# Kernel optimization log

Measured on AMD Instinct MI355X. Metric: run time of the kernel, lower is better.

Reference implementation:

```python
import jax, jax.numpy as jnp
import numpy as np

DIM = 1024
HEADS = 16
DIM_HEAD = DIM // HEADS

def setup_inputs() -> dict:
    key = jax.random.key(0)
    k1, k2, k3 = jax.random.split(key, 3)
    x = jax.random.normal(k1, (2, 2048, DIM), dtype=jnp.float32)
    # nn.Linear(dim, 3*dim, bias=False): weight [3*dim, dim]; y = x @ W.T
    W_qkv = jax.random.normal(k2, (3 * DIM, DIM), dtype=jnp.float32) * (1.0 / np.sqrt(DIM))
    W_out = jax.random.normal(k3, (DIM, DIM), dtype=jnp.float32) * (1.0 / np.sqrt(DIM))
    return {"x": x, "W_qkv": W_qkv, "W_out": W_out}

def reference(x, W_qkv, W_out):
    b, s, _ = x.shape
    scale = DIM_HEAD ** -0.5
    qkv = x @ W_qkv.T                              # [b, s, 3*dim]
    q, k, v = jnp.split(qkv, 3, axis=-1)
    def to_heads(t):
        return t.reshape(b, s, HEADS, DIM_HEAD).transpose(0, 2, 1, 3)  # [b,h,s,d]
    q, k, v = map(to_heads, (q, k, v))
    scores = jnp.einsum('bhid,bhjd->bhij', q, k) * scale
    causal_mask = jnp.triu(jnp.ones((s, s), dtype=bool), k=1)
    scores = jnp.where(causal_mask, -jnp.inf, scores)
    attn = jax.nn.softmax(scores, axis=-1)
    out = jnp.einsum('bhij,bhjd->bhid', attn, v)
    out = out.transpose(0, 2, 1, 3).reshape(b, s, HEADS * DIM_HEAD)
    return out @ W_out.T
```

## Files before the change

### kernel.cpp

```cpp
#include <hip/hip_runtime.h>
#include <hip/hip_bf16.h>
#include <math.h>

using bf16 = __hip_bfloat16;
typedef __attribute__((ext_vector_type(8))) short bf16x8;
typedef __attribute__((ext_vector_type(4))) short bf16x4;
typedef __attribute__((ext_vector_type(4))) float f32x4;

static __device__ __forceinline__ void gl_lds16(const void* g, void* l) {
  __builtin_amdgcn_global_load_lds(
      (const __attribute__((address_space(1))) unsigned int*)g,
      (__attribute__((address_space(3))) unsigned int*)l, 16, 0, 0);
}

#define MFMA16 __builtin_amdgcn_mfma_f32_16x16x32_bf16
#define MFMA16K16 __builtin_amdgcn_mfma_f32_16x16x16bf16_1k

static __device__ __forceinline__ short f2bf(float f) {
  return (short)((__builtin_bit_cast(unsigned int, f) + 0x8000u) >> 16);
}

__global__ __launch_bounds__(256) void cvt_f32_bf16(
    const float* __restrict__ in, bf16* __restrict__ out) {
  const int i = (blockIdx.x * 256 + threadIdx.x) * 4;
  const float4 v = *(const float4*)(in + i);
  bf16x4 o;
  o.x = (short)__builtin_bit_cast(unsigned short, __float2bfloat16(v.x));
  o.y = (short)__builtin_bit_cast(unsigned short, __float2bfloat16(v.y));
  o.z = (short)__builtin_bit_cast(unsigned short, __float2bfloat16(v.z));
  o.w = (short)__builtin_bit_cast(unsigned short, __float2bfloat16(v.w));
  *(bf16x4*)(out + i) = o;
}

template <int K>
static __device__ __forceinline__ void gemm_bt_acc(
    const bf16* __restrict__ A, const bf16* __restrict__ B,
    int rowA0, int rowB0, bf16* As, bf16* Bs, f32x4 acc[4][4]) {
  const int t = threadIdx.x;
  const int w = t >> 6, l = t & 63;
  const int quad = l >> 4, l16 = l & 15;
  const int wm = (w >> 1) * 64, wn = (w & 1) * 64;
  const int c0 = t, c1 = t + 256;
  const bf16* a0 = A + (size_t)(rowA0 + (c0 >> 2)) * K + (c0 & 3) * 8;
  const bf16* a1 = A + (size_t)(rowA0 + (c1 >> 2)) * K + (c1 & 3) * 8;
  const bf16* b0 = B + (size_t)(rowB0 + (c0 >> 2)) * K + (c0 & 3) * 8;
  const bf16* b1 = B + (size_t)(rowB0 + (c1 >> 2)) * K + (c1 & 3) * 8;
  for (int k0 = 0; k0 < K; k0 += 32) {
    __syncthreads();
    gl_lds16(a0 + k0, As + c0 * 8);
    gl_lds16(a1 + k0, As + c1 * 8);
    gl_lds16(b0 + k0, Bs + c0 * 8);
    gl_lds16(b1 + k0, Bs + c1 * 8);
    __syncthreads();
    bf16x8 af[4], bg[4];
#pragma unroll
    for (int i = 0; i < 4; i++)
      af[i] = *(const bf16x8*)(As + (wm + i * 16 + l16) * 32 + quad * 8);
#pragma unroll
    for (int j = 0; j < 4; j++)
      bg[j] = *(const bf16x8*)(Bs + (wn + j * 16 + l16) * 32 + quad * 8);
#pragma unroll
    for (int i = 0; i < 4; i++)
#pragma unroll
      for (int j = 0; j < 4; j++)
        acc[i][j] = MFMA16(af[i], bg[j], acc[i][j], 0, 0, 0);
  }
}

__global__ __launch_bounds__(256) void qkv_gemm(
    const bf16* __restrict__ x, const bf16* __restrict__ Wqkv,
    bf16* __restrict__ Qb, bf16* __restrict__ Kb, bf16* __restrict__ Vt) {
  __shared__ bf16 As[128 * 32];
  __shared__ bf16 Bs[128 * 32];
  f32x4 acc[4][4];
#pragma unroll
  for (int i = 0; i < 4; i++)
#pragma unroll
    for (int j = 0; j < 4; j++) acc[i][j] = (f32x4){0.f, 0.f, 0.f, 0.f};
  const int bm = blockIdx.x, bn = blockIdx.y;
  gemm_bt_acc<1024>(x, Wqkv, bm * 128, bn * 128, As, Bs, acc);

  const int t = threadIdx.x, w = t >> 6, l = t & 63;
  const int quad = l >> 4, l16 = l & 15;
  const int wm = (w >> 1) * 64, wn = (w & 1) * 64;
#pragma unroll
  for (int i = 0; i < 4; i++) {
#pragma unroll
    for (int j = 0; j < 4; j++) {
      const int n = bn * 128 + wn + j * 16 + l16;
      const int which = n >> 10;
      const int nn = n & 1023;
      const int h = nn >> 6, d = nn & 63;
#pragma unroll
      for (int r = 0; r < 4; r++) {
        const int m = bm * 128 + wm + i * 16 + quad * 4 + r;
        const int b = m >> 11, s = m & 2047;
        const int bh = b * 16 + h;
        const bf16 v = __float2bfloat16(acc[i][j][r]);
        if (which == 0)
          Qb[((size_t)bh * 2048 + s) * 64 + d] = v;
        else if (which == 1)
          Kb[((size_t)bh * 2048 + s) * 64 + d] = v;
        else
          Vt[((size_t)bh * 64 + d) * 2048 + s] = v;
      }
    }
  }
}

__global__ __launch_bounds__(256) void attn_kernel(
    const bf16* __restrict__ Qb, const bf16* __restrict__ Kb,
    const bf16* __restrict__ Vt, bf16* __restrict__ attn) {
  __shared__ bf16 Qs[64 * 64];
  __shared__ bf16 Ks[64 * 64];
  __shared__ bf16 Vts[64 * 64];
  const int x = blockIdx.x;
  const int bh = x & 31;
  const int idx = x >> 5;
  const int qt = (idx < 16) ? idx : 47 - idx;
  const int q0 = qt * 64;
  const int t = threadIdx.x, w = t >> 6, l = t & 63;
  const int quad = l >> 4, l16 = l & 15;
  const float c_exp2 = 0.18033688011f;

  const bf16* Qg = Qb + ((size_t)bh * 2048 + q0) * 64;
#pragma unroll
  for (int c = t; c < 512; c += 256) {
    const int row = c >> 3, pos = c & 7;
    gl_lds16(Qg + (row * 8 + (pos ^ (row & 7))) * 8, Qs + c * 8);
  }

  f32x4 oacc[4];
  float lsum = 0.f;
#pragma unroll
  for (int md = 0; md < 4; md++) oacc[md] = (f32x4){0.f, 0.f, 0.f, 0.f};

  const int nj = qt + 1;
  for (int j = 0; j < nj; j++) {
    const int j0 = j * 64;
    __syncthreads();
    const bf16* Kg = Kb + ((size_t)bh * 2048 + j0) * 64;
#pragma unroll
    for (int c = t; c < 512; c += 256) {
      const int row = c >> 3, pos = c & 7;
      gl_lds16(Kg + (row * 8 + (pos ^ (row & 7))) * 8, Ks + c * 8);
    }
    const bf16* Vg = Vt + (size_t)bh * 64 * 2048 + j0;
#pragma unroll
    for (int c = t; c < 512; c += 256) {
      const int d = c >> 3, pos = c & 7;
      gl_lds16(Vg + (size_t)d * 2048 + ((pos ^ (d & 7)) * 8), Vts + c * 8);
    }
    __syncthreads();

    f32x4 sacc[4];
#pragma unroll
    for (int mt = 0; mt < 4; mt++) sacc[mt] = (f32x4){0.f, 0.f, 0.f, 0.f};
#pragma unroll
    for (int kk = 0; kk < 2; kk++) {
      const int qrow = w * 16 + l16;
      const int qpos = (kk * 4 + quad) ^ (qrow & 7);
      bf16x8 qf = *(const bf16x8*)(Qs + qrow * 64 + qpos * 8);
#pragma unroll
      for (int mt = 0; mt < 4; mt++) {
        const int row = mt * 16 + l16;
        const int pos = (kk * 4 + quad) ^ (row & 7);
        bf16x8 kf = *(const bf16x8*)(Ks + row * 64 + pos * 8);
        sacc[mt] = MFMA16(kf, qf, sacc[mt], 0, 0, 0);
      }
    }

    bf16x4 pfrag[4];
#pragma unroll
    for (int mt = 0; mt < 4; mt++) {
      bf16x4 p4;
#pragma unroll
      for (int r = 0; r < 4; r++) {
        float p = exp2f(sacc[mt][r] * c_exp2);
        if (j == qt) {
          const int sg = j0 + mt * 16 + quad * 4 + r;
          const int qi = q0 + w * 16 + l16;
          if (sg > qi) p = 0.f;
        }
        lsum += p;
        p4[r] = f2bf(p);
      }
      pfrag[mt] = p4;
    }

#pragma unroll
    for (int kt = 0; kt < 4; kt++) {
#pragma unroll
      for (int md = 0; md < 4; md++) {
        const int d = md * 16 + l16;
        const int pos = (kt * 2 + (quad >> 1)) ^ (d & 7);
        bf16x4 va = *(const bf16x4*)(Vts + d * 64 + pos * 8 + (quad & 1) * 4);
        oacc[md] = MFMA16K16(va, pfrag[kt], oacc[md], 0, 0, 0);
      }
    }
  }

  lsum += __shfl_xor(lsum, 16, 64);
  lsum += __shfl_xor(lsum, 32, 64);
  const float inv = 1.0f / lsum;
  const int b = bh >> 4, h = bh & 15;
  const int srow = q0 + w * 16 + l16;
#pragma unroll
  for (int md = 0; md < 4; md++) {
    bf16x4 o4;
#pragma unroll
    for (int r = 0; r < 4; r++)
      o4[r] = (short)__builtin_bit_cast(
          unsigned short, __float2bfloat16(oacc[md][r] * inv));
    *(bf16x4*)(attn + ((size_t)b * 2048 + srow) * 1024 + h * 64 + md * 16 +
               quad * 4) = o4;
  }
}

__global__ __launch_bounds__(256) void out_gemm(
    const bf16* __restrict__ attn, const bf16* __restrict__ Wout,
    float* __restrict__ out) {
  __shared__ bf16 As[128 * 32];
  __shared__ bf16 Bs[128 * 32];
  f32x4 acc[4][4];
#pragma unroll
  for (int i = 0; i < 4; i++)
#pragma unroll
    for (int j = 0; j < 4; j++) acc[i][j] = (f32x4){0.f, 0.f, 0.f, 0.f};
  const int bm = blockIdx.x, bn = blockIdx.y;
  gemm_bt_acc<1024>(attn, Wout, bm * 128, bn * 128, As, Bs, acc);

  const int t = threadIdx.x, w = t >> 6, l = t & 63;
  const int quad = l >> 4, l16 = l & 15;
  const int wm = (w >> 1) * 64, wn = (w & 1) * 64;
#pragma unroll
  for (int i = 0; i < 4; i++) {
#pragma unroll
    for (int j = 0; j < 4; j++) {
      const int n = bn * 128 + wn + j * 16 + l16;
#pragma unroll
      for (int r = 0; r < 4; r++) {
        const int m = bm * 128 + wm + i * 16 + quad * 4 + r;
        out[(size_t)m * 1024 + n] = acc[i][j][r];
      }
    }
  }
}

extern "C" void kernel_launch(void* const* d_in, const int* in_sizes, int n_in,
                              void* d_out, int out_size, void* d_ws, size_t ws_size,
                              hipStream_t stream) {
  const float* x = (const float*)d_in[0];
  const float* Wqkv = (const float*)d_in[1];
  const float* Wout = (const float*)d_in[2];
  float* out = (float*)d_out;

  char* ws = (char*)d_ws;
  const size_t MB = 1024 * 1024;
  bf16* xb = (bf16*)(ws + 0 * MB);
  bf16* at = (bf16*)(ws + 0 * MB);
  bf16* Wqkvb = (bf16*)(ws + 8 * MB);
  bf16* Woutb = (bf16*)(ws + 14 * MB);
  bf16* Qb = (bf16*)(ws + 16 * MB);
  bf16* Kb = (bf16*)(ws + 24 * MB);
  bf16* Vt = (bf16*)(ws + 32 * MB);

  cvt_f32_bf16<<<4096, 256, 0, stream>>>(x, xb);
  cvt_f32_bf16<<<3072, 256, 0, stream>>>(Wqkv, Wqkvb);
  cvt_f32_bf16<<<1024, 256, 0, stream>>>(Wout, Woutb);

  qkv_gemm<<<dim3(32, 24), 256, 0, stream>>>(xb, Wqkvb, Qb, Kb, Vt);
  attn_kernel<<<1024, 256, 0, stream>>>(Qb, Kb, Vt, at);
  out_gemm<<<dim3(32, 8), 256, 0, stream>>>(at, Woutb, out);
}
```

Before: 183.7 us.

## Widen attention KV tile to 128 and merge conversion kernels into one launch

```diff
diff --git a/kernel.cpp b/kernel.cpp
--- a/kernel.cpp
+++ b/kernel.cpp
@@ -20,16 +20,29 @@
   return (short)((__builtin_bit_cast(unsigned int, f) + 0x8000u) >> 16);
 }
 
-__global__ __launch_bounds__(256) void cvt_f32_bf16(
-    const float* __restrict__ in, bf16* __restrict__ out) {
-  const int i = (blockIdx.x * 256 + threadIdx.x) * 4;
-  const float4 v = *(const float4*)(in + i);
+__global__ __launch_bounds__(256) void cvt_all(
+    const float* __restrict__ x, const float* __restrict__ wqkv,
+    const float* __restrict__ wout, bf16* __restrict__ xb,
+    bf16* __restrict__ wqkvb, bf16* __restrict__ woutb) {
+  const int blk = blockIdx.x;
+  const float* src;
+  bf16* dst;
+  int base;
+  if (blk < 4096) {
+    src = x; dst = xb; base = blk;
+  } else if (blk < 7168) {
+    src = wqkv; dst = wqkvb; base = blk - 4096;
+  } else {
+    src = wout; dst = woutb; base = blk - 7168;
+  }
+  const int i = (base * 256 + threadIdx.x) * 4;
+  const float4 v = *(const float4*)(src + i);
   bf16x4 o;
-  o.x = (short)__builtin_bit_cast(unsigned short, __float2bfloat16(v.x));
-  o.y = (short)__builtin_bit_cast(unsigned short, __float2bfloat16(v.y));
-  o.z = (short)__builtin_bit_cast(unsigned short, __float2bfloat16(v.z));
-  o.w = (short)__builtin_bit_cast(unsigned short, __float2bfloat16(v.w));
-  *(bf16x4*)(out + i) = o;
+  o.x = f2bf(v.x);
+  o.y = f2bf(v.y);
+  o.z = f2bf(v.z);
+  o.w = f2bf(v.w);
+  *(bf16x4*)(dst + i) = o;
 }
 
 template <int K>
@@ -112,8 +125,8 @@
     const bf16* __restrict__ Qb, const bf16* __restrict__ Kb,
     const bf16* __restrict__ Vt, bf16* __restrict__ attn) {
   __shared__ bf16 Qs[64 * 64];
-  __shared__ bf16 Ks[64 * 64];
-  __shared__ bf16 Vts[64 * 64];
+  __shared__ bf16 Ks[128 * 64];
+  __shared__ bf16 Vts[64 * 128];
   const int x = blockIdx.x;
   const int bh = x & 31;
   const int idx = x >> 5;
@@ -135,34 +148,34 @@
 #pragma unroll
   for (int md = 0; md < 4; md++) oacc[md] = (f32x4){0.f, 0.f, 0.f, 0.f};
 
-  const int nj = qt + 1;
-  for (int j = 0; j < nj; j++) {
-    const int j0 = j * 64;
+  const int njj = (qt + 2) >> 1;
+  for (int jj = 0; jj < njj; jj++) {
+    const int j0 = jj * 128;
     __syncthreads();
     const bf16* Kg = Kb + ((size_t)bh * 2048 + j0) * 64;
 #pragma unroll
-    for (int c = t; c < 512; c += 256) {
+    for (int c = t; c < 1024; c += 256) {
       const int row = c >> 3, pos = c & 7;
       gl_lds16(Kg + (row * 8 + (pos ^ (row & 7))) * 8, Ks + c * 8);
     }
     const bf16* Vg = Vt + (size_t)bh * 64 * 2048 + j0;
 #pragma unroll
-    for (int c = t; c < 512; c += 256) {
-      const int d = c >> 3, pos = c & 7;
-      gl_lds16(Vg + (size_t)d * 2048 + ((pos ^ (d & 7)) * 8), Vts + c * 8);
-    }
-    __syncthreads();
-
-    f32x4 sacc[4];
-#pragma unroll
-    for (int mt = 0; mt < 4; mt++) sacc[mt] = (f32x4){0.f, 0.f, 0.f, 0.f};
+    for (int c = t; c < 1024; c += 256) {
+      const int d = c >> 4, pos = c & 15;
+      gl_lds16(Vg + (size_t)d * 2048 + ((pos ^ (d & 15)) * 8), Vts + c * 8);
+    }
+    __syncthreads();
+
+    f32x4 sacc[8];
+#pragma unroll
+    for (int mt = 0; mt < 8; mt++) sacc[mt] = (f32x4){0.f, 0.f, 0.f, 0.f};
 #pragma unroll
     for (int kk = 0; kk < 2; kk++) {
       const int qrow = w * 16 + l16;
       const int qpos = (kk * 4 + quad) ^ (qrow & 7);
       bf16x8 qf = *(const bf16x8*)(Qs + qrow * 64 + qpos * 8);
 #pragma unroll
-      for (int mt = 0; mt < 4; mt++) {
+      for (int mt = 0; mt < 8; mt++) {
         const int row = mt * 16 + l16;
         const int pos = (kk * 4 + quad) ^ (row & 7);
         bf16x8 kf = *(const bf16x8*)(Ks + row * 64 + pos * 8);
@@ -170,31 +183,42 @@
       }
     }
 
-    bf16x4 pfrag[4];
-#pragma unroll
-    for (int mt = 0; mt < 4; mt++) {
-      bf16x4 p4;
-#pragma unroll
-      for (int r = 0; r < 4; r++) {
-        float p = exp2f(sacc[mt][r] * c_exp2);
-        if (j == qt) {
+    bf16x4 pfrag[8];
+    if (jj == njj - 1) {
+      const int qi = q0 + w * 16 + l16;
+#pragma unroll
+      for (int mt = 0; mt < 8; mt++) {
+        bf16x4 p4;
+#pragma unroll
+        for (int r = 0; r < 4; r++) {
           const int sg = j0 + mt * 16 + quad * 4 + r;
-          const int qi = q0 + w * 16 + l16;
-          if (sg > qi) p = 0.f;
+          float p = (sg <= qi) ? exp2f(sacc[mt][r] * c_exp2) : 0.f;
+          lsum += p;
+          p4[r] = f2bf(p);
         }
-        lsum += p;
-        p4[r] = f2bf(p);
-      }
-      pfrag[mt] = p4;
-    }
-
-#pragma unroll
-    for (int kt = 0; kt < 4; kt++) {
+        pfrag[mt] = p4;
+      }
+    } else {
+#pragma unroll
+      for (int mt = 0; mt < 8; mt++) {
+        bf16x4 p4;
+#pragma unroll
+        for (int r = 0; r < 4; r++) {
+          const float p = exp2f(sacc[mt][r] * c_exp2);
+          lsum += p;
+          p4[r] = f2bf(p);
+        }
+        pfrag[mt] = p4;
+      }
+    }
+
+#pragma unroll
+    for (int kt = 0; kt < 8; kt++) {
 #pragma unroll
       for (int md = 0; md < 4; md++) {
         const int d = md * 16 + l16;
-        const int pos = (kt * 2 + (quad >> 1)) ^ (d & 7);
-        bf16x4 va = *(const bf16x4*)(Vts + d * 64 + pos * 8 + (quad & 1) * 4);
+        const int pos = (kt * 2 + (quad >> 1)) ^ (d & 15);
+        bf16x4 va = *(const bf16x4*)(Vts + d * 128 + pos * 8 + (quad & 1) * 4);
         oacc[md] = MFMA16K16(va, pfrag[kt], oacc[md], 0, 0, 0);
       }
     }
@@ -209,9 +233,7 @@
   for (int md = 0; md < 4; md++) {
     bf16x4 o4;
 #pragma unroll
-    for (int r = 0; r < 4; r++)
-      o4[r] = (short)__builtin_bit_cast(
-          unsigned short, __float2bfloat16(oacc[md][r] * inv));
+    for (int r = 0; r < 4; r++) o4[r] = f2bf(oacc[md][r] * inv);
     *(bf16x4*)(attn + ((size_t)b * 2048 + srow) * 1024 + h * 64 + md * 16 +
                quad * 4) = o4;
   }
@@ -265,10 +287,7 @@
   bf16* Kb = (bf16*)(ws + 24 * MB);
   bf16* Vt = (bf16*)(ws + 32 * MB);
 
-  cvt_f32_bf16<<<4096, 256, 0, stream>>>(x, xb);
-  cvt_f32_bf16<<<3072, 256, 0, stream>>>(Wqkv, Wqkvb);
-  cvt_f32_bf16<<<1024, 256, 0, stream>>>(Wout, Woutb);
-
+  cvt_all<<<8192, 256, 0, stream>>>(x, Wqkv, Wout, xb, Wqkvb, Woutb);
   qkv_gemm<<<dim3(32, 24), 256, 0, stream>>>(xb, Wqkvb, Qb, Kb, Vt);
   attn_kernel<<<1024, 256, 0, stream>>>(Qb, Kb, Vt, at);
   out_gemm<<<dim3(32, 8), 256, 0, stream>>>(at, Woutb, out);
```

New measurement: 182.5 us. About the same (-0.7%).
